# Kernel tuning notes

Hardware: AMD Instinct MI355X
Metric: run time of the kernel (lower is better)

The kernel has to match this reference:

```python
import jax, jax.numpy as jnp
import numpy as np

GROUPS = 12
POOL = 64
TOPK = 8
LAYERS = 24
RANK = 64
HID = 1024


def setup_inputs() -> dict:
    key = jax.random.key(0)
    k1, k2, k3 = jax.random.split(key, 3)
    queries = jax.random.normal(k1, (64, 768), dtype=jnp.float32)
    keys = jax.random.normal(k2, (1, GROUPS, POOL, 768 // GROUPS), dtype=jnp.float32)
    weight_offset = jax.random.normal(
        k3, (POOL, 2, HID * RANK * LAYERS), dtype=jnp.float32
    )
    return {"queries": queries, "keys": keys, "weight_offset": weight_offset}


def reference(queries, keys, weight_offset):
    # queries: [b, g*c] -> [b, g, c]
    b = queries.shape[0]
    q = queries.reshape(b, GROUPS, -1)
    # cosine similarity against pool keys: sim [b, g, pool]
    qn = q / jnp.clip(jnp.linalg.norm(q, axis=-1, keepdims=True), 1e-8)
    kn = keys[0] / jnp.clip(jnp.linalg.norm(keys[0], axis=-1, keepdims=True), 1e-8)
    sim = jnp.einsum("bgc,gpc->bgp", qn, kn)
    # routing uses detached similarities (sim.clone().detach())
    idx_sim = jax.lax.stop_gradient(sim)
    # use_distance_weight=True path: mean over batch and groups -> [pool]
    mean_sim = jnp.mean(idx_sim, axis=(0, 1))
    dis_weight, idx_vote = jax.lax.top_k(mean_sim, TOPK)
    dis_weight = dis_weight / (dis_weight.sum() + 1e-9)
    # gather top-k low-rank factors: [k, 2, D]
    wo = weight_offset[idx_vote]
    low_rank_a = wo[:, 0, :].reshape(TOPK, LAYERS, RANK, HID)
    low_rank_b = wo[:, 1, :].reshape(TOPK, LAYERS, RANK, HID)
    # [k, L, H, H] low-rank outer products
    offset = jnp.einsum("nlrx,nlry->nlxy", low_rank_a, low_rank_b)
    # distance-weighted combine -> [L, H, H]
    weight_offset_out = jnp.einsum("n,nlxy->lxy", dis_weight, offset)
    return weight_offset_out
```

## Files before the change

kernel.cpp:

```cpp
#include <hip/hip_runtime.h>
#include <hip/hip_bf16.h>

#define GROUPS 12
#define POOL   64
#define TOPK   8
#define LAYERS 24
#define RANK   64
#define HID    1024
#define D_LR   (HID * RANK * LAYERS)
#define POOL_STRIDE (2L * D_LR)

typedef __attribute__((ext_vector_type(8))) short bf16x8;
typedef __attribute__((ext_vector_type(4))) float f32x4;

__device__ __forceinline__ unsigned bfpack2(float lo, float hi) {
    float2 t; t.x = lo; t.y = hi;
    union { __hip_bfloat162 h; unsigned u; } cv;
    cv.h = __float22bfloat162_rn(t);
    return cv.u;
}

__device__ __forceinline__ int sw_idx(int col, int chunk) {
    return chunk ^ (col & 7) ^ ((col >> 2) & 7);
}

__global__ void routing_kernel(const float* __restrict__ q,
                               const float* __restrict__ keys,
                               int* __restrict__ idx_out,
                               float* __restrict__ w_out) {
    __shared__ float invn[64][GROUPS];
    __shared__ float qbar[GROUPS][64];
    __shared__ float simg[GROUPS][64];
    const int t = threadIdx.x;

    {
        int b = t / GROUPS, g = t % GROUPS;
        const float* row = q + b * 768 + g * 64;
        float ss = 0.f;
        #pragma unroll 8
        for (int c = 0; c < 64; ++c) { float v = row[c]; ss = fmaf(v, v, ss); }
        invn[b][g] = 1.f / fmaxf(sqrtf(ss), 1e-8f);
    }
    __syncthreads();
    {
        int g = t >> 6, c = t & 63;
        float s = 0.f;
        for (int b = 0; b < 64; ++b) s = fmaf(q[b * 768 + g * 64 + c], invn[b][g], s);
        qbar[g][c] = s;
    }
    __syncthreads();
    {
        int g = t >> 6, p = t & 63;
        const float* krow = keys + (g * 64 + p) * 64;
        float ss = 0.f, dot = 0.f;
        #pragma unroll 8
        for (int c = 0; c < 64; ++c) {
            float v = krow[c];
            ss  = fmaf(v, v, ss);
            dot = fmaf(v, qbar[g][c], dot);
        }
        simg[g][p] = dot / fmaxf(sqrtf(ss), 1e-8f);
    }
    __syncthreads();
    if (t < 64) {
        float s = 0.f;
        for (int g = 0; g < GROUPS; ++g) s += simg[g][t];
        qbar[0][t] = s * (1.f / 768.f);
    }
    __syncthreads();
    if (t == 0) {
        float ms[POOL];
        for (int p = 0; p < POOL; ++p) ms[p] = qbar[0][p];
        float sum = 0.f;
        float vals[TOPK]; int ids[TOPK];
        for (int k = 0; k < TOPK; ++k) {
            float best = -3.4e38f; int bi = 0;
            for (int p = 0; p < POOL; ++p)
                if (ms[p] > best) { best = ms[p]; bi = p; }
            vals[k] = best; ids[k] = bi;
            ms[bi] = -3.4e38f; sum += best;
        }
        float inv = 1.f / (sum + 1e-9f);
        for (int k = 0; k < TOPK; ++k) { idx_out[k] = ids[k]; w_out[k] = vals[k] * inv; }
    }
}

__global__ __launch_bounds__(512, 2) void lowrank_mfma_kernel(
        const float* __restrict__ wo,
        const int*   __restrict__ idx,
        const float* __restrict__ w,
        float*       __restrict__ out)
{
    __shared__ uint4 As4[256][8];
    __shared__ uint4 Bs4[256][8];
    __shared__ int   s_idx[TOPK];
    __shared__ float s_w[TOPK];

    const int tid = threadIdx.x;
    const int d    = blockIdx.x;
    const int orig = (d & 7) * 48 + (d >> 3);
    const int l    = orig >> 4;
    const int rem  = orig & 15;
    const int m0   = (rem >> 2) * 256;
    const int n0   = (rem & 3) * 256;

    if (tid < TOPK) { s_idx[tid] = idx[tid]; s_w[tid] = w[tid]; }
    __syncthreads();

    const int lane = tid & 63;
    const int wave = tid >> 6;
    const int wr = wave >> 2;
    const int wc = wave & 3;
    const int fr = lane & 15;
    const int kb = lane >> 4;

    const int c4 = lane;
    const int rg = wave;

    f32x4 acc[8][4];
    #pragma unroll
    for (int i = 0; i < 8; ++i)
        #pragma unroll
        for (int j = 0; j < 4; ++j) acc[i][j] = (f32x4){0.f, 0.f, 0.f, 0.f};

    f32x4 araw[8], braw[8];

    auto load_raw = [&](int s) {
        const long base = (long)s_idx[s] * POOL_STRIDE + (long)l * (RANK * HID);
        const float* pa = wo + base + (long)(rg * 8) * HID + (m0 + c4 * 4);
        const float* pb = wo + base + D_LR + (long)(rg * 8) * HID + (n0 + c4 * 4);
        #pragma unroll
        for (int j = 0; j < 8; ++j) araw[j] = *(const f32x4*)(pa + (long)j * HID);
        #pragma unroll
        for (int j = 0; j < 8; ++j) braw[j] = *(const f32x4*)(pb + (long)j * HID);
    };

    load_raw(0);

    for (int s = 0; s < 8; ++s) {
        const float wn = s_w[s];
        #pragma unroll
        for (int cc = 0; cc < 4; ++cc) {
            const int col = c4 * 4 + cc;
            uint4 ua, ub;
            ua.x = bfpack2(wn * araw[0][cc], wn * araw[1][cc]);
            ua.y = bfpack2(wn * araw[2][cc], wn * araw[3][cc]);
            ua.z = bfpack2(wn * araw[4][cc], wn * araw[5][cc]);
            ua.w = bfpack2(wn * araw[6][cc], wn * araw[7][cc]);
            ub.x = bfpack2(braw[0][cc], braw[1][cc]);
            ub.y = bfpack2(braw[2][cc], braw[3][cc]);
            ub.z = bfpack2(braw[4][cc], braw[5][cc]);
            ub.w = bfpack2(braw[6][cc], braw[7][cc]);
            const int cp = sw_idx(col, rg);
            As4[col][cp] = ua;
            Bs4[col][cp] = ub;
        }
        __syncthreads();

        if (s < 7) load_raw(s + 1);

        #pragma unroll
        for (int kk = 0; kk < 2; ++kk) {
            const int chunk = kk * 4 + kb;
            bf16x8 bfv[4];
            #pragma unroll
            for (int fj = 0; fj < 4; ++fj) {
                const int n = wc * 64 + fj * 16 + fr;
                bfv[fj] = *(const bf16x8*)&Bs4[n][sw_idx(n, chunk)];
            }
            #pragma unroll
            for (int fi = 0; fi < 8; ++fi) {
                const int m = wr * 128 + fi * 16 + fr;
                const bf16x8 af = *(const bf16x8*)&As4[m][sw_idx(m, chunk)];
                #pragma unroll
                for (int fj = 0; fj < 4; ++fj)
                    acc[fi][fj] = __builtin_amdgcn_mfma_f32_16x16x32_bf16(
                        af, bfv[fj], acc[fi][fj], 0, 0, 0);
            }
        }
        __syncthreads();
    }

    float* o = out + (long)l * (1024 * 1024);
    #pragma unroll
    for (int fi = 0; fi < 8; ++fi) {
        #pragma unroll
        for (int fj = 0; fj < 4; ++fj) {
            const int n = n0 + wc * 64 + fj * 16 + fr;
            #pragma unroll
            for (int v = 0; v < 4; ++v) {
                const int m = m0 + wr * 128 + fi * 16 + kb * 4 + v;
                o[(long)m * 1024 + n] = acc[fi][fj][v];
            }
        }
    }
}

extern "C" void kernel_launch(void* const* d_in, const int* in_sizes, int n_in,
                              void* d_out, int out_size, void* d_ws, size_t ws_size,
                              hipStream_t stream) {
    const float* q    = (const float*)d_in[0];
    const float* keys = (const float*)d_in[1];
    const float* wo   = (const float*)d_in[2];
    float* out = (float*)d_out;

    int*   idx = (int*)d_ws;
    float* w   = (float*)((char*)d_ws + 32);

    routing_kernel<<<1, 768, 0, stream>>>(q, keys, idx, w);

    lowrank_mfma_kernel<<<dim3(384, 1, 1), 512, 0, stream>>>(wo, idx, w, out);
}
```

Before: 82.96 us.

## Use persistent 256-block grid with second-tile prefetch for low-rank GEMM

Reduces the grid from 384 to 256 blocks so that half the blocks process two output tiles sequentially, with an XCD-aware tile mapping. The raw loads for the second tile are issued during the last k-stage of the first tile, and accumulators are reset after each tile's store. This aims to avoid the partial second wave of the 1.5-wave launch, at the cost of serialising two tiles on some blocks.

```diff
diff --git a/kernel.cpp b/kernel.cpp
--- a/kernel.cpp
+++ b/kernel.cpp
@@ -97,12 +97,13 @@
     __shared__ float s_w[TOPK];
 
     const int tid = threadIdx.x;
-    const int d    = blockIdx.x;
-    const int orig = (d & 7) * 48 + (d >> 3);
-    const int l    = orig >> 4;
-    const int rem  = orig & 15;
-    const int m0   = (rem >> 2) * 256;
-    const int n0   = (rem & 3) * 256;
+    const int b   = blockIdx.x;
+    const int xcd = b & 7;
+    const int i   = b >> 3;
+
+    const int tile0 = (2 * xcd + (i >> 4)) * 16 + (i & 15);
+    const int nt    = (i < 16) ? 2 : 1;
+    const int tile1 = (16 + xcd) * 16 + i;
 
     if (tid < TOPK) { s_idx[tid] = idx[tid]; s_w[tid] = w[tid]; }
     __syncthreads();
@@ -119,13 +120,17 @@
 
     f32x4 acc[8][4];
     #pragma unroll
-    for (int i = 0; i < 8; ++i)
-        #pragma unroll
-        for (int j = 0; j < 4; ++j) acc[i][j] = (f32x4){0.f, 0.f, 0.f, 0.f};
+    for (int p = 0; p < 8; ++p)
+        #pragma unroll
+        for (int q2 = 0; q2 < 4; ++q2) acc[p][q2] = (f32x4){0.f, 0.f, 0.f, 0.f};
 
     f32x4 araw[8], braw[8];
 
-    auto load_raw = [&](int s) {
+    auto load_raw = [&](int T, int s) {
+        const int l   = T >> 4;
+        const int rem = T & 15;
+        const int m0  = (rem >> 2) * 256;
+        const int n0  = (rem & 3) * 256;
         const long base = (long)s_idx[s] * POOL_STRIDE + (long)l * (RANK * HID);
         const float* pa = wo + base + (long)(rg * 8) * HID + (m0 + c4 * 4);
         const float* pb = wo + base + D_LR + (long)(rg * 8) * HID + (n0 + c4 * 4);
@@ -135,62 +140,72 @@
         for (int j = 0; j < 8; ++j) braw[j] = *(const f32x4*)(pb + (long)j * HID);
     };
 
-    load_raw(0);
-
-    for (int s = 0; s < 8; ++s) {
-        const float wn = s_w[s];
-        #pragma unroll
-        for (int cc = 0; cc < 4; ++cc) {
-            const int col = c4 * 4 + cc;
-            uint4 ua, ub;
-            ua.x = bfpack2(wn * araw[0][cc], wn * araw[1][cc]);
-            ua.y = bfpack2(wn * araw[2][cc], wn * araw[3][cc]);
-            ua.z = bfpack2(wn * araw[4][cc], wn * araw[5][cc]);
-            ua.w = bfpack2(wn * araw[6][cc], wn * araw[7][cc]);
-            ub.x = bfpack2(braw[0][cc], braw[1][cc]);
-            ub.y = bfpack2(braw[2][cc], braw[3][cc]);
-            ub.z = bfpack2(braw[4][cc], braw[5][cc]);
-            ub.w = bfpack2(braw[6][cc], braw[7][cc]);
-            const int cp = sw_idx(col, rg);
-            As4[col][cp] = ua;
-            Bs4[col][cp] = ub;
-        }
-        __syncthreads();
-
-        if (s < 7) load_raw(s + 1);
-
-        #pragma unroll
-        for (int kk = 0; kk < 2; ++kk) {
-            const int chunk = kk * 4 + kb;
-            bf16x8 bfv[4];
+    load_raw(tile0, 0);
+
+    for (int ti = 0; ti < nt; ++ti) {
+        const int T   = (ti == 0) ? tile0 : tile1;
+        const int l   = T >> 4;
+        const int rem = T & 15;
+        const int m0  = (rem >> 2) * 256;
+        const int n0  = (rem & 3) * 256;
+
+        for (int s = 0; s < 8; ++s) {
+            const float wn = s_w[s];
+            #pragma unroll
+            for (int cc = 0; cc < 4; ++cc) {
+                const int col = c4 * 4 + cc;
+                uint4 ua, ub;
+                ua.x = bfpack2(wn * araw[0][cc], wn * araw[1][cc]);
+                ua.y = bfpack2(wn * araw[2][cc], wn * araw[3][cc]);
+                ua.z = bfpack2(wn * araw[4][cc], wn * araw[5][cc]);
+                ua.w = bfpack2(wn * araw[6][cc], wn * araw[7][cc]);
+                ub.x = bfpack2(braw[0][cc], braw[1][cc]);
+                ub.y = bfpack2(braw[2][cc], braw[3][cc]);
+                ub.z = bfpack2(braw[4][cc], braw[5][cc]);
+                ub.w = bfpack2(braw[6][cc], braw[7][cc]);
+                const int cp = sw_idx(col, rg);
+                As4[col][cp] = ua;
+                Bs4[col][cp] = ub;
+            }
+            __syncthreads();
+
+            if (s < 7)            load_raw(T, s + 1);
+            else if (ti + 1 < nt) load_raw(tile1, 0);
+
+            #pragma unroll
+            for (int kk = 0; kk < 2; ++kk) {
+                const int chunk = kk * 4 + kb;
+                bf16x8 bfv[4];
+                #pragma unroll
+                for (int fj = 0; fj < 4; ++fj) {
+                    const int n = wc * 64 + fj * 16 + fr;
+                    bfv[fj] = *(const bf16x8*)&Bs4[n][sw_idx(n, chunk)];
+                }
+                #pragma unroll
+                for (int fi = 0; fi < 8; ++fi) {
+                    const int m = wr * 128 + fi * 16 + fr;
+                    const bf16x8 af = *(const bf16x8*)&As4[m][sw_idx(m, chunk)];
+                    #pragma unroll
+                    for (int fj = 0; fj < 4; ++fj)
+                        acc[fi][fj] = __builtin_amdgcn_mfma_f32_16x16x32_bf16(
+                            af, bfv[fj], acc[fi][fj], 0, 0, 0);
+                }
+            }
+            __syncthreads();
+        }
+
+        float* o = out + (long)l * (1024 * 1024);
+        #pragma unroll
+        for (int fi = 0; fi < 8; ++fi) {
             #pragma unroll
             for (int fj = 0; fj < 4; ++fj) {
-                const int n = wc * 64 + fj * 16 + fr;
-                bfv[fj] = *(const bf16x8*)&Bs4[n][sw_idx(n, chunk)];
-            }
-            #pragma unroll
-            for (int fi = 0; fi < 8; ++fi) {
-                const int m = wr * 128 + fi * 16 + fr;
-                const bf16x8 af = *(const bf16x8*)&As4[m][sw_idx(m, chunk)];
+                const int n = n0 + wc * 64 + fj * 16 + fr;
                 #pragma unroll
-                for (int fj = 0; fj < 4; ++fj)
-                    acc[fi][fj] = __builtin_amdgcn_mfma_f32_16x16x32_bf16(
-                        af, bfv[fj], acc[fi][fj], 0, 0, 0);
-            }
-        }
-        __syncthreads();
-    }
-
-    float* o = out + (long)l * (1024 * 1024);
-    #pragma unroll
-    for (int fi = 0; fi < 8; ++fi) {
-        #pragma unroll
-        for (int fj = 0; fj < 4; ++fj) {
-            const int n = n0 + wc * 64 + fj * 16 + fr;
-            #pragma unroll
-            for (int v = 0; v < 4; ++v) {
-                const int m = m0 + wr * 128 + fi * 16 + kb * 4 + v;
-                o[(long)m * 1024 + n] = acc[fi][fj][v];
+                for (int v = 0; v < 4; ++v) {
+                    const int m = m0 + wr * 128 + fi * 16 + kb * 4 + v;
+                    o[(long)m * 1024 + n] = acc[fi][fj][v];
+                }
+                acc[fi][fj] = (f32x4){0.f, 0.f, 0.f, 0.f};
             }
         }
     }
@@ -209,5 +224,5 @@
 
     routing_kernel<<<1, 768, 0, stream>>>(q, keys, idx, w);
 
-    lowrank_mfma_kernel<<<dim3(384, 1, 1), 512, 0, stream>>>(wo, idx, w, out);
-}
+    lowrank_mfma_kernel<<<dim3(256, 1, 1), 512, 0, stream>>>(wo, idx, w, out);
+}
```

Result: faster. 80.14 us (median of 2 runs) (-3.4%).

## Widen output tile to 256x512 per block and halve grid size

Applied to the files above, without the earlier changes.

Each block now computes a 256x512 output tile instead of 256x256, so each wave holds 8x8 MFMA accumulators and the grid shrinks from 384 to 192 blocks. The block-to-tile mapping is rewritten so each XCD handles three contiguous layers, which keeps A/B reuse local to that XCD. The intent is to cut redundant global loads of the A factors and the per-tile conversion work. In exchange, register pressure doubles (acc 64 vectors plus 16 raw B vectors), which threatens the 2-blocks-per-CU launch bound and can cause spills, and 192 blocks may underfill the 256 CUs.

```diff
diff --git a/kernel.cpp b/kernel.cpp
--- a/kernel.cpp
+++ b/kernel.cpp
@@ -92,17 +92,19 @@
         float*       __restrict__ out)
 {
     __shared__ uint4 As4[256][8];
-    __shared__ uint4 Bs4[256][8];
+    __shared__ uint4 Bs4[512][8];
     __shared__ int   s_idx[TOPK];
     __shared__ float s_w[TOPK];
 
     const int tid = threadIdx.x;
-    const int d    = blockIdx.x;
-    const int orig = (d & 7) * 48 + (d >> 3);
-    const int l    = orig >> 4;
-    const int rem  = orig & 15;
-    const int m0   = (rem >> 2) * 256;
-    const int n0   = (rem & 3) * 256;
+    const int b   = blockIdx.x;
+    const int xcd = b & 7;
+    const int i   = b >> 3;
+
+    const int l   = 3 * xcd + (i >> 3);
+    const int pos = i & 7;
+    const int m0  = (pos >> 1) * 256;
+    const int n0  = (pos & 1) * 512;
 
     if (tid < TOPK) { s_idx[tid] = idx[tid]; s_w[tid] = w[tid]; }
     __syncthreads();
@@ -114,25 +116,28 @@
     const int fr = lane & 15;
     const int kb = lane >> 4;
 
-    const int c4 = lane;
-    const int rg = wave;
-
-    f32x4 acc[8][4];
+    const int c4a = lane;
+    const int rga = wave;
+    const int c4b = (tid & 127);
+    const int rgb = tid >> 7;
+
+    f32x4 acc[8][8];
     #pragma unroll
-    for (int i = 0; i < 8; ++i)
-        #pragma unroll
-        for (int j = 0; j < 4; ++j) acc[i][j] = (f32x4){0.f, 0.f, 0.f, 0.f};
-
-    f32x4 araw[8], braw[8];
+    for (int p = 0; p < 8; ++p)
+        #pragma unroll
+        for (int q2 = 0; q2 < 8; ++q2) acc[p][q2] = (f32x4){0.f, 0.f, 0.f, 0.f};
+
+    f32x4 araw[8];
+    f32x4 braw[16];
 
     auto load_raw = [&](int s) {
         const long base = (long)s_idx[s] * POOL_STRIDE + (long)l * (RANK * HID);
-        const float* pa = wo + base + (long)(rg * 8) * HID + (m0 + c4 * 4);
-        const float* pb = wo + base + D_LR + (long)(rg * 8) * HID + (n0 + c4 * 4);
-        #pragma unroll
-        for (int j = 0; j < 8; ++j) araw[j] = *(const f32x4*)(pa + (long)j * HID);
-        #pragma unroll
-        for (int j = 0; j < 8; ++j) braw[j] = *(const f32x4*)(pb + (long)j * HID);
+        const float* pa = wo + base + (long)(rga * 8) * HID + (m0 + c4a * 4);
+        const float* pb = wo + base + D_LR + (long)(rgb * 16) * HID + (n0 + c4b * 4);
+        #pragma unroll
+        for (int j = 0; j < 8; ++j)  araw[j] = *(const f32x4*)(pa + (long)j * HID);
+        #pragma unroll
+        for (int j = 0; j < 16; ++j) braw[j] = *(const f32x4*)(pb + (long)j * HID);
     };
 
     load_raw(0);
@@ -141,19 +146,28 @@
         const float wn = s_w[s];
         #pragma unroll
         for (int cc = 0; cc < 4; ++cc) {
-            const int col = c4 * 4 + cc;
-            uint4 ua, ub;
+            const int col = c4a * 4 + cc;
+            uint4 ua;
             ua.x = bfpack2(wn * araw[0][cc], wn * araw[1][cc]);
             ua.y = bfpack2(wn * araw[2][cc], wn * araw[3][cc]);
             ua.z = bfpack2(wn * araw[4][cc], wn * araw[5][cc]);
             ua.w = bfpack2(wn * araw[6][cc], wn * araw[7][cc]);
-            ub.x = bfpack2(braw[0][cc], braw[1][cc]);
-            ub.y = bfpack2(braw[2][cc], braw[3][cc]);
-            ub.z = bfpack2(braw[4][cc], braw[5][cc]);
-            ub.w = bfpack2(braw[6][cc], braw[7][cc]);
-            const int cp = sw_idx(col, rg);
-            As4[col][cp] = ua;
-            Bs4[col][cp] = ub;
+            As4[col][sw_idx(col, rga)] = ua;
+        }
+        #pragma unroll
+        for (int cc = 0; cc < 4; ++cc) {
+            const int col = c4b * 4 + cc;
+            uint4 u0, u1;
+            u0.x = bfpack2(braw[0][cc],  braw[1][cc]);
+            u0.y = bfpack2(braw[2][cc],  braw[3][cc]);
+            u0.z = bfpack2(braw[4][cc],  braw[5][cc]);
+            u0.w = bfpack2(braw[6][cc],  braw[7][cc]);
+            u1.x = bfpack2(braw[8][cc],  braw[9][cc]);
+            u1.y = bfpack2(braw[10][cc], braw[11][cc]);
+            u1.z = bfpack2(braw[12][cc], braw[13][cc]);
+            u1.w = bfpack2(braw[14][cc], braw[15][cc]);
+            Bs4[col][sw_idx(col, 2 * rgb)]     = u0;
+            Bs4[col][sw_idx(col, 2 * rgb + 1)] = u1;
         }
         __syncthreads();
 
@@ -162,20 +176,20 @@
         #pragma unroll
         for (int kk = 0; kk < 2; ++kk) {
             const int chunk = kk * 4 + kb;
-            bf16x8 bfv[4];
-            #pragma unroll
-            for (int fj = 0; fj < 4; ++fj) {
-                const int n = wc * 64 + fj * 16 + fr;
-                bfv[fj] = *(const bf16x8*)&Bs4[n][sw_idx(n, chunk)];
-            }
+            bf16x8 af[8];
             #pragma unroll
             for (int fi = 0; fi < 8; ++fi) {
                 const int m = wr * 128 + fi * 16 + fr;
-                const bf16x8 af = *(const bf16x8*)&As4[m][sw_idx(m, chunk)];
+                af[fi] = *(const bf16x8*)&As4[m][sw_idx(m, chunk)];
+            }
+            #pragma unroll
+            for (int fj = 0; fj < 8; ++fj) {
+                const int n = wc * 128 + fj * 16 + fr;
+                const bf16x8 bv = *(const bf16x8*)&Bs4[n][sw_idx(n, chunk)];
                 #pragma unroll
-                for (int fj = 0; fj < 4; ++fj)
+                for (int fi = 0; fi < 8; ++fi)
                     acc[fi][fj] = __builtin_amdgcn_mfma_f32_16x16x32_bf16(
-                        af, bfv[fj], acc[fi][fj], 0, 0, 0);
+                        af[fi], bv, acc[fi][fj], 0, 0, 0);
             }
         }
         __syncthreads();
@@ -185,8 +199,8 @@
     #pragma unroll
     for (int fi = 0; fi < 8; ++fi) {
         #pragma unroll
-        for (int fj = 0; fj < 4; ++fj) {
-            const int n = n0 + wc * 64 + fj * 16 + fr;
+        for (int fj = 0; fj < 8; ++fj) {
+            const int n = n0 + wc * 128 + fj * 16 + fr;
             #pragma unroll
             for (int v = 0; v < 4; ++v) {
                 const int m = m0 + wr * 128 + fi * 16 + kb * 4 + v;
@@ -209,5 +223,5 @@
 
     routing_kernel<<<1, 768, 0, stream>>>(q, keys, idx, w);
 
-    lowrank_mfma_kernel<<<dim3(384, 1, 1), 512, 0, stream>>>(wo, idx, w, out);
-}
+    lowrank_mfma_kernel<<<dim3(192, 1, 1), 512, 0, stream>>>(wo, idx, w, out);
+}
```

Result: slower. 267.5 us (+222.4%).
